# Performance work log

Measured on AMD Instinct MI355X. Metric: run time of the kernel, lower is better.

Reference implementation:

```python
import jax, jax.numpy as jnp
import numpy as np

NUM_LAYERS = 2
HIDDEN = 512
INPUT = 512


def _lstm_cell(x, h, c, Wih, Whh, bih, bbh):
    # PyTorch LSTMCell: gates ordered i, f, g, o
    g = x @ Wih.T + bih + h @ Whh.T + bbh  # [B, 4H]
    i, f, gg, o = jnp.split(g, 4, axis=-1)
    c_new = jax.nn.sigmoid(f) * c + jax.nn.sigmoid(i) * jnp.tanh(gg)
    h_new = jax.nn.sigmoid(o) * jnp.tanh(c_new)
    return h_new, c_new


def setup_inputs() -> dict:
    key = jax.random.key(0)
    ks = jax.random.split(key, 8)
    B, T = 64, 512
    s = 1.0 / np.sqrt(HIDDEN)
    return {
        "x": jax.random.normal(ks[0], (B, T, INPUT), dtype=jnp.float32),
        "h0": jax.random.normal(ks[1], (NUM_LAYERS, B, HIDDEN), dtype=jnp.float32),
        "c0": jax.random.normal(ks[2], (NUM_LAYERS, B, HIDDEN), dtype=jnp.float32),
        # stacked per-layer weights (input_size == hidden_size so shapes match)
        "W_ih": jax.random.uniform(ks[3], (NUM_LAYERS, 4 * HIDDEN, INPUT), jnp.float32, -s, s),
        "W_hh": jax.random.uniform(ks[4], (NUM_LAYERS, 4 * HIDDEN, HIDDEN), jnp.float32, -s, s),
        "b_ih": jax.random.uniform(ks[5], (NUM_LAYERS, 4 * HIDDEN), jnp.float32, -s, s),
        "b_hh": jax.random.uniform(ks[6], (NUM_LAYERS, 4 * HIDDEN), jnp.float32, -s, s),
    }


def reference(x, h0, c0, W_ih, W_hh, b_ih, b_hh):
    # x: [B, T, D]; h0/c0: [L, B, H]
    xs = jnp.swapaxes(x, 0, 1)  # [T, B, D] for scan over time

    def step(carry, x_t):
        h, c = carry  # each [L, B, H]
        h_list, c_list = [], []
        inp = x_t
        for j in range(NUM_LAYERS):  # small static unroll over layers
            h_j, c_j = _lstm_cell(inp, h[j], c[j], W_ih[j], W_hh[j], b_ih[j], b_hh[j])
            h_list.append(h_j)
            c_list.append(c_j)
            inp = h_j
        h_new = jnp.stack(h_list, axis=0)
        c_new = jnp.stack(c_list, axis=0)
        return (h_new, c_new), inp  # output of top layer

    (h_fin, c_fin), outs = jax.lax.scan(step, (h0, c0), xs)
    out = jnp.swapaxes(outs, 0, 1)  # [B, T, H]
    return out, h_fin, c_fin
```

## Files before the change

kernel.cpp:

```cpp
#include <hip/hip_runtime.h>
#include <hip/hip_bf16.h>


#define TT 512

using short8 = __attribute__((ext_vector_type(8))) short;
using f32x4  = __attribute__((ext_vector_type(4))) float;

__device__ __forceinline__ short f2bf(float f) {
  unsigned u = __float_as_uint(f);
  u = (u + 0x7fffu + ((u >> 16) & 1u)) >> 16;
  return (short)u;
}
__device__ __forceinline__ float bf2f(short s) {
  return __uint_as_float(((unsigned)(unsigned short)s) << 16);
}
__device__ __forceinline__ float sigf(float x) { return 1.f / (1.f + __expf(-x)); }
__device__ __forceinline__ float tanh_(float x) { return 1.f - 2.f / (__expf(2.f * x) + 1.f); }

__device__ __forceinline__ void ld8_nw(short8* d,
    const short* p0, const short* p1, const short* p2, const short* p3,
    const short* p4, const short* p5, const short* p6, const short* p7) {
  asm volatile(
      "global_load_dwordx4 %0, %8, off sc0\n\t"
      "global_load_dwordx4 %1, %9, off sc0\n\t"
      "global_load_dwordx4 %2, %10, off sc0\n\t"
      "global_load_dwordx4 %3, %11, off sc0\n\t"
      "global_load_dwordx4 %4, %12, off sc0\n\t"
      "global_load_dwordx4 %5, %13, off sc0\n\t"
      "global_load_dwordx4 %6, %14, off sc0\n\t"
      "global_load_dwordx4 %7, %15, off sc0"
      : "=&v"(d[0]), "=&v"(d[1]), "=&v"(d[2]), "=&v"(d[3]),
        "=&v"(d[4]), "=&v"(d[5]), "=&v"(d[6]), "=&v"(d[7])
      : "v"(p0), "v"(p1), "v"(p2), "v"(p3),
        "v"(p4), "v"(p5), "v"(p6), "v"(p7)
      : "memory");
}

#define TIE8(A, CNT)                                                        \
  asm volatile(CNT : "+v"(A[0]), "+v"(A[1]), "+v"(A[2]), "+v"(A[3]),        \
                     "+v"(A[4]), "+v"(A[5]), "+v"(A[6]), "+v"(A[7])         \
               ::"memory")

__device__ __forceinline__ void stc_short(short* p, short v) {
  asm volatile("global_store_short %0, %1, off sc0 sc1"
               :: "v"(p), "v"((int)v) : "memory");
}
__device__ __forceinline__ void stc_float(float* p, float v) {
  asm volatile("global_store_dword %0, %1, off sc0 sc1"
               :: "v"(p), "v"(v) : "memory");
}

__device__ __forceinline__ void l2inv() {
  asm volatile("buffer_inv sc1" ::: "memory");
}

__global__ __launch_bounds__(256) void conv_x(const float* __restrict__ x,
                                              short* __restrict__ xo) {
  size_t g = (size_t)blockIdx.x * 256 + threadIdx.x;
  size_t i = g * 8;
  float4 v0 = *(const float4*)(x + i);
  float4 v1 = *(const float4*)(x + i + 4);
  short8 r;
  r[0] = f2bf(v0.x); r[1] = f2bf(v0.y); r[2] = f2bf(v0.z); r[3] = f2bf(v0.w);
  r[4] = f2bf(v1.x); r[5] = f2bf(v1.y); r[6] = f2bf(v1.z); r[7] = f2bf(v1.w);
  *(short8*)(xo + (i >> 9) * 1024 + (i & 511)) = r;
}

__global__ __launch_bounds__(256) void conv_w(const float* __restrict__ Wih,
                                              const float* __restrict__ Whh,
                                              short* __restrict__ wp) {
  int g = blockIdx.x * 256 + threadIdx.x;
  int l = g / 393216;
  int rem = g % 393216;
  int j8 = rem / 6144;
  int q8 = rem % 6144;
  int s, hl, bt, c, lane;
  if (q8 < 2048) {
    s = 0; hl = 0;
    int seg = q8 >> 6; bt = seg >> 4; c = seg & 15; lane = q8 & 63;
  } else {
    int q = q8 - 2048;
    s = 1;
    int seg = q >> 6; bt = seg >> 5; c = (seg >> 1) & 15; hl = seg & 1;
    lane = q & 63;
  }
  int r = lane & 15;
  int gg = r >> 2, jj = r & 3;
  int R = gg * 512 + j8 * 8 + bt * 4 + jj;
  int k = c * 32 + (lane >> 4) * 8;
  const float* src = (s ? Whh : Wih) + ((size_t)(l * 2048 + R)) * 512 + k;
  short8 o;
#pragma unroll
  for (int e = 0; e < 8; ++e) {
    float v = src[e];
    short hi = f2bf(v);
    o[e] = hl ? f2bf(v - bf2f(hi)) : hi;
  }
  *(short8*)(wp + (size_t)g * 8) = o;
}

__global__ __launch_bounds__(256) void init_state(const float* __restrict__ h0,
                                                  short* __restrict__ hhi,
                                                  short* __restrict__ hlo,
                                                  unsigned* __restrict__ bar) {
  int i = blockIdx.x * 256 + threadIdx.x;
  int l = i >> 15, bj = i & 32767;
  int b = bj >> 9, j = bj & 511;
  float h = h0[i];
  short hi = f2bf(h);
  int slot = l ? 5 : 3;
  int o = slot * 32768 + (j >> 3) * 512 + b * 8 + (j & 7);
  hhi[o] = hi;
  hlo[o] = f2bf(h - bf2f(hi));
  if (blockIdx.x < 8) bar[blockIdx.x * 256 + threadIdx.x] = 0u;
}

__device__ __forceinline__ void garrive(unsigned* cnt, int tid, int slot) {
  __syncthreads();
  if (tid == 0)
    __hip_atomic_fetch_add(&cnt[slot * 32], 1u, __ATOMIC_RELAXED,
                           __HIP_MEMORY_SCOPE_AGENT);
}
__device__ __forceinline__ void gwait1(unsigned* c1, unsigned t1, int tid) {
  if (tid == 0) {
    for (;;) {
      unsigned s1 = 0;
#pragma unroll
      for (int r = 0; r < 32; ++r)
        s1 += __hip_atomic_load(&c1[r * 32], __ATOMIC_RELAXED,
                                __HIP_MEMORY_SCOPE_AGENT);
      if (s1 >= t1) break;
      __builtin_amdgcn_s_sleep(1);
    }
  }
  __syncthreads();
  if (tid < 64) l2inv();
  __syncthreads();
}
__device__ __forceinline__ void gwait2(unsigned* c1, unsigned t1,
                                       unsigned* c2, unsigned t2, int tid) {
  if (tid == 0) {
    for (;;) {
      unsigned s1 = 0, s2 = 0;
#pragma unroll
      for (int r = 0; r < 32; ++r) {
        s1 += __hip_atomic_load(&c1[r * 32], __ATOMIC_RELAXED,
                                __HIP_MEMORY_SCOPE_AGENT);
        s2 += __hip_atomic_load(&c2[r * 32], __ATOMIC_RELAXED,
                                __HIP_MEMORY_SCOPE_AGENT);
      }
      if (s1 >= t1 && s2 >= t2) break;
      __builtin_amdgcn_s_sleep(1);
    }
  }
  __syncthreads();
  if (tid < 64) l2inv();
  __syncthreads();
}

__global__ __launch_bounds__(512, 1) void lstm_persist(
    const short* __restrict__ wp, const float* __restrict__ c0,
    const float* __restrict__ bih, const float* __restrict__ bhh,
    short* __restrict__ hhi, short* __restrict__ hlo,
    unsigned* __restrict__ bar, float* __restrict__ out) {
  extern __shared__ char smem[];
  short* lw = (short*)smem;
  float* sG = (float*)(smem + 98304);

  const int tid = threadIdx.x;
  const int layer = blockIdx.x >> 6;
  const int j8 = blockIdx.x & 63;
  const int bslot = blockIdx.x & 31;
  unsigned* cntMy = bar + (layer << 10);
  unsigned* cntOt = bar + ((layer ^ 1) << 10);
  const int wv = tid >> 6;
  const int kq = wv & 3;
  const int ah = wv >> 2;
  const int lane = tid & 63;
  const int m = lane & 15;
  const int koq = lane >> 4;
  const int cbase = kq << 2;

  {
    const short* src = wp + (size_t)(layer * 64 + j8) * 49152;
    for (int i = tid; i < 6144; i += 512)
      *(short8*)(lw + i * 8) = *(const short8*)(src + i * 8);
  }

  const int sb = tid >> 3, sj = tid & 7;
  const int j = (j8 << 3) + sj;
  float creg = c0[layer * 32768 + sb * 512 + j];
  float hf = 0.f;
  float bsum[4];
#pragma unroll
  for (int g = 0; g < 4; ++g)
    bsum[g] = bih[layer * 2048 + g * 512 + j] + bhh[layer * 2048 + g * 512 + j];
  __syncthreads();

  const int br0 = ((ah * 2 + 0) << 4) + m;
  const int br1 = ((ah * 2 + 1) << 4) + m;
  const short* xo = (const short*)out;

  f32x4 acc[2][2];

  auto zacc = [&]() {
#pragma unroll
    for (int u = 0; u < 2; ++u)
#pragma unroll
      for (int v = 0; v < 2; ++v) acc[u][v] = f32x4{0.f, 0.f, 0.f, 0.f};
  };

#define PA(rX, cc, br) \
  ((rX) + ((((cbase + (cc)) << 2) + koq) << 9) + (br) * 8)

  auto ih_l0 = [&](int txt) {
#pragma unroll
    for (int cc = 0; cc < 4; ++cc) {
      const int c = cbase + cc;
      const int k = c * 32 + (koq << 3);
      short8 b0 = *(const short8*)(lw + c * 512 + lane * 8);
      short8 b1 = *(const short8*)(lw + (16 + c) * 512 + lane * 8);
#pragma unroll
      for (int it = 0; it < 2; ++it) {
        const int br = it ? br1 : br0;
        short8 a = *(const short8*)(xo + ((size_t)br * TT + txt) * 1024 + k);
        acc[0][it] = __builtin_amdgcn_mfma_f32_16x16x32_bf16(a, b0, acc[0][it], 0, 0, 0);
        acc[1][it] = __builtin_amdgcn_mfma_f32_16x16x32_bf16(a, b1, acc[1][it], 0, 0, 0);
      }
    }
  };

  auto ih_l1 = [&](const short* ph) {
    short8 Ax[8];
    ld8_nw(Ax, PA(ph, 0, br0), PA(ph, 0, br1), PA(ph, 1, br0), PA(ph, 1, br1),
               PA(ph, 2, br0), PA(ph, 2, br1), PA(ph, 3, br0), PA(ph, 3, br1));
    TIE8(Ax, "s_waitcnt vmcnt(0)");
#pragma unroll
    for (int cc = 0; cc < 4; ++cc) {
      const int c = cbase + cc;
      short8 b0 = *(const short8*)(lw + c * 512 + lane * 8);
      short8 b1 = *(const short8*)(lw + (16 + c) * 512 + lane * 8);
#pragma unroll
      for (int it = 0; it < 2; ++it) {
        short8 a = Ax[cc * 2 + it];
        acc[0][it] = __builtin_amdgcn_mfma_f32_16x16x32_bf16(a, b0, acc[0][it], 0, 0, 0);
        acc[1][it] = __builtin_amdgcn_mfma_f32_16x16x32_bf16(a, b1, acc[1][it], 0, 0, 0);
      }
    }
  };

  auto stepBody = [&](const short* rh, const short* rl, int slotOut, int t) {
    short8 Ah[8], Al[8];
    ld8_nw(Ah, PA(rh, 0, br0), PA(rh, 0, br1), PA(rh, 1, br0), PA(rh, 1, br1),
               PA(rh, 2, br0), PA(rh, 2, br1), PA(rh, 3, br0), PA(rh, 3, br1));
    ld8_nw(Al, PA(rl, 0, br0), PA(rl, 0, br1), PA(rl, 1, br0), PA(rl, 1, br1),
               PA(rl, 2, br0), PA(rl, 2, br1), PA(rl, 3, br0), PA(rl, 3, br1));
    TIE8(Ah, "s_waitcnt vmcnt(0)");
    TIE8(Al, "");

#pragma unroll
    for (int cc = 0; cc < 4; ++cc) {
      const int c = cbase + cc;
      short8 bh0 = *(const short8*)(lw + 16384 + (c * 2 + 0) * 512 + lane * 8);
      short8 bl0 = *(const short8*)(lw + 16384 + (c * 2 + 1) * 512 + lane * 8);
      short8 bh1 = *(const short8*)(lw + 16384 + ((16 + c) * 2 + 0) * 512 + lane * 8);
      short8 bl1 = *(const short8*)(lw + 16384 + ((16 + c) * 2 + 1) * 512 + lane * 8);
#pragma unroll
      for (int it = 0; it < 2; ++it) {
        short8 a = Ah[cc * 2 + it];
        short8 al = Al[cc * 2 + it];
        acc[0][it] = __builtin_amdgcn_mfma_f32_16x16x32_bf16(a, bh0, acc[0][it], 0, 0, 0);
        acc[0][it] = __builtin_amdgcn_mfma_f32_16x16x32_bf16(a, bl0, acc[0][it], 0, 0, 0);
        acc[0][it] = __builtin_amdgcn_mfma_f32_16x16x32_bf16(al, bh0, acc[0][it], 0, 0, 0);
        acc[1][it] = __builtin_amdgcn_mfma_f32_16x16x32_bf16(a, bh1, acc[1][it], 0, 0, 0);
        acc[1][it] = __builtin_amdgcn_mfma_f32_16x16x32_bf16(a, bl1, acc[1][it], 0, 0, 0);
        acc[1][it] = __builtin_amdgcn_mfma_f32_16x16x32_bf16(al, bh1, acc[1][it], 0, 0, 0);
      }
    }

#pragma unroll
    for (int bt = 0; bt < 2; ++bt)
#pragma unroll
      for (int it = 0; it < 2; ++it) {
        const int srow = bt * 16 + m;
        const int col = ((ah * 2 + it) << 4) + (koq << 2);
#pragma unroll
        for (int r = 0; r < 4; ++r)
          sG[(kq * 32 + srow) * 66 + col + r] = acc[bt][it][r];
      }
    __syncthreads();

    {
      const int bt = sj >> 2, jl = sj & 3;
      float gv[4];
#pragma unroll
      for (int g = 0; g < 4; ++g) {
        const int s = bt * 16 + g * 4 + jl;
        gv[g] = sG[(0 * 32 + s) * 66 + sb] + sG[(1 * 32 + s) * 66 + sb] +
                sG[(2 * 32 + s) * 66 + sb] + sG[(3 * 32 + s) * 66 + sb] +
                bsum[g];
      }
      const float cn = sigf(gv[1]) * creg + sigf(gv[0]) * tanh_(gv[2]);
      const float hn = sigf(gv[3]) * tanh_(cn);
      creg = cn;
      hf = hn;
      const int ho = slotOut * 32768 + (j8 << 9) + tid;
      const short hb = f2bf(hn);
      stc_short(hhi + ho, hb);
      stc_short(hlo + ho, f2bf(hn - bf2f(hb)));
      if (layer)
        stc_float(&out[((size_t)sb * 512 + t) * 512 + j], hn);
    }
  };

  if (layer == 0) {
    zacc();
    ih_l0(0);
    for (int t = 0; t < TT; ++t) {
      if (t >= 4)
        gwait2(cntMy, (unsigned)(64 * t), cntOt, (unsigned)(64 * (t - 3)), tid);
      else if (t >= 1)
        gwait1(cntMy, (unsigned)(64 * t), tid);
      const int ps = (t + 3) & 3;
      stepBody(hhi + ps * 32768, hlo + ps * 32768, t & 3, t);
      garrive(cntMy, tid, bslot);
      if (t + 1 < TT) {
        zacc();
        ih_l0(t + 1);
      }
    }
  } else {
    zacc();
    gwait1(cntOt, 64u, tid);
    ih_l1(hhi + 0 * 32768);
    for (int t = 0; t < TT; ++t) {
      if (t >= 1) gwait1(cntMy, (unsigned)(64 * t), tid);
      const int ps = 4 + ((t + 1) & 1);
      stepBody(hhi + ps * 32768, hlo + ps * 32768, 4 + (t & 1), t);
      garrive(cntMy, tid, bslot);
      if (t + 1 < TT) {
        gwait1(cntOt, (unsigned)(64 * (t + 2)), tid);
        zacc();
        ih_l1(hhi + ((t + 1) & 3) * 32768);
      }
    }
  }

  stc_float(&out[16777216 + layer * 32768 + sb * 512 + j], hf);
  stc_float(&out[16777216 + 65536 + layer * 32768 + sb * 512 + j], creg);
}


extern "C" void kernel_launch(void* const* d_in, const int* in_sizes, int n_in,
                              void* d_out, int out_size, void* d_ws,
                              size_t ws_size, hipStream_t stream) {
  const float* x = (const float*)d_in[0];
  const float* h0 = (const float*)d_in[1];
  const float* c0 = (const float*)d_in[2];
  const float* Wih = (const float*)d_in[3];
  const float* Whh = (const float*)d_in[4];
  const float* bih = (const float*)d_in[5];
  const float* bhh = (const float*)d_in[6];
  float* out = (float*)d_out;

  char* ws = (char*)d_ws;
  short* wp = (short*)(ws + 0);
  short* hhi = (short*)(ws + 12582912);
  short* hlo = (short*)(ws + 12976128);
  unsigned* bar = (unsigned*)(ws + 13369344);

  hipFuncSetAttribute(reinterpret_cast<const void*>(lstm_persist),
                      hipFuncAttributeMaxDynamicSharedMemorySize, 132096);

  conv_x<<<8192, 256, 0, stream>>>(x, (short*)out);
  conv_w<<<3072, 256, 0, stream>>>(Wih, Whh, wp);
  init_state<<<256, 256, 0, stream>>>(h0, hhi, hlo, bar);

  void* args[] = {(void*)&wp,  (void*)&c0,  (void*)&bih, (void*)&bhh,
                  (void*)&hhi, (void*)&hlo, (void*)&bar, (void*)&out};
  hipLaunchCooperativeKernel(reinterpret_cast<void*>(lstm_persist), dim3(128),
                             dim3(512), args, 132096, stream);
}
```

Measured before the change: 3.153 ms.

## Elect one leader block per XCC to invalidate L2 and signal peers via flags

```diff
diff --git a/kernel.cpp b/kernel.cpp
--- a/kernel.cpp
+++ b/kernel.cpp
@@ -51,8 +51,8 @@
                :: "v"(p), "v"(v) : "memory");
 }
 
-__device__ __forceinline__ void l2inv() {
-  asm volatile("buffer_inv sc1" ::: "memory");
+__device__ __forceinline__ void l2inv_wait() {
+  asm volatile("buffer_inv sc1\n\ts_waitcnt vmcnt(0)" ::: "memory");
 }
 
 __global__ __launch_bounds__(256) void conv_x(const float* __restrict__ x,
@@ -113,7 +113,16 @@
   int o = slot * 32768 + (j >> 3) * 512 + b * 8 + (j & 7);
   hhi[o] = hi;
   hlo[o] = f2bf(h - bf2f(hi));
-  if (blockIdx.x < 8) bar[blockIdx.x * 256 + threadIdx.x] = 0u;
+  if (blockIdx.x < 16) bar[blockIdx.x * 256 + threadIdx.x] = 0u;
+}
+
+__device__ __forceinline__ unsigned csum(unsigned* c) {
+  unsigned s = 0;
+#pragma unroll
+  for (int r = 0; r < 32; ++r)
+    s += __hip_atomic_load(&c[r * 32], __ATOMIC_RELAXED,
+                           __HIP_MEMORY_SCOPE_AGENT);
+  return s;
 }
 
 __device__ __forceinline__ void garrive(unsigned* cnt, int tid, int slot) {
@@ -122,40 +131,41 @@
     __hip_atomic_fetch_add(&cnt[slot * 32], 1u, __ATOMIC_RELAXED,
                            __HIP_MEMORY_SCOPE_AGENT);
 }
-__device__ __forceinline__ void gwait1(unsigned* c1, unsigned t1, int tid) {
+
+__device__ __forceinline__ void gw_main(unsigned* c1, unsigned t1,
+                                        unsigned* c2, unsigned t2, int tid,
+                                        bool lead, unsigned* flg, unsigned ft) {
   if (tid == 0) {
     for (;;) {
-      unsigned s1 = 0;
-#pragma unroll
-      for (int r = 0; r < 32; ++r)
-        s1 += __hip_atomic_load(&c1[r * 32], __ATOMIC_RELAXED,
-                                __HIP_MEMORY_SCOPE_AGENT);
-      if (s1 >= t1) break;
+      bool ok = (csum(c1) >= t1);
+      if (c2) ok = ok && (csum(c2) >= t2);
+      if (ok) break;
       __builtin_amdgcn_s_sleep(1);
     }
+    if (lead) {
+      l2inv_wait();
+      __hip_atomic_store(flg, ft, __ATOMIC_RELAXED, __HIP_MEMORY_SCOPE_AGENT);
+    } else {
+      while (__hip_atomic_load(flg, __ATOMIC_RELAXED,
+                               __HIP_MEMORY_SCOPE_AGENT) < ft)
+        __builtin_amdgcn_s_sleep(1);
+    }
   }
   __syncthreads();
-  if (tid < 64) l2inv();
-  __syncthreads();
-}
-__device__ __forceinline__ void gwait2(unsigned* c1, unsigned t1,
-                                       unsigned* c2, unsigned t2, int tid) {
+}
+
+__device__ __forceinline__ void gw_other(unsigned* c, unsigned tc, int tid,
+                                         unsigned* flg, unsigned ft) {
   if (tid == 0) {
-    for (;;) {
-      unsigned s1 = 0, s2 = 0;
-#pragma unroll
-      for (int r = 0; r < 32; ++r) {
-        s1 += __hip_atomic_load(&c1[r * 32], __ATOMIC_RELAXED,
-                                __HIP_MEMORY_SCOPE_AGENT);
-        s2 += __hip_atomic_load(&c2[r * 32], __ATOMIC_RELAXED,
-                                __HIP_MEMORY_SCOPE_AGENT);
-      }
-      if (s1 >= t1 && s2 >= t2) break;
-      __builtin_amdgcn_s_sleep(1);
-    }
-  }
-  __syncthreads();
-  if (tid < 64) l2inv();
+    while (csum(c) < tc) __builtin_amdgcn_s_sleep(1);
+    if (flg) {
+      while (__hip_atomic_load(flg, __ATOMIC_RELAXED,
+                               __HIP_MEMORY_SCOPE_AGENT) < ft)
+        __builtin_amdgcn_s_sleep(1);
+    } else {
+      l2inv_wait();
+    }
+  }
   __syncthreads();
 }
 
@@ -172,8 +182,11 @@
   const int layer = blockIdx.x >> 6;
   const int j8 = blockIdx.x & 63;
   const int bslot = blockIdx.x & 31;
-  unsigned* cntMy = bar + (layer << 10);
-  unsigned* cntOt = bar + ((layer ^ 1) << 10);
+  unsigned* cnt0 = bar;
+  unsigned* cnt1 = bar + 1024;
+  unsigned* icnt = bar + 2048;
+  unsigned* claim = bar + 2080;
+  unsigned* flags = bar + 2176;
   const int wv = tid >> 6;
   const int kq = wv & 3;
   const int ah = wv >> 2;
@@ -182,6 +195,18 @@
   const int koq = lane >> 4;
   const int cbase = kq << 2;
 
+  int xcc;
+  asm volatile("s_getreg_b32 %0, hwreg(HW_REG_XCC_ID)" : "=s"(xcc));
+  xcc &= 15;
+  bool lead = false;
+  if (tid == 0)
+    lead = (__hip_atomic_fetch_add(&claim[layer * 16 + xcc], 1u,
+                                   __ATOMIC_RELAXED,
+                                   __HIP_MEMORY_SCOPE_AGENT) == 0u);
+  if (tid == 0)
+    __hip_atomic_fetch_add(icnt, 1u, __ATOMIC_RELAXED,
+                           __HIP_MEMORY_SCOPE_AGENT);
+
   {
     const short* src = wp + (size_t)(layer * 64 + j8) * 49152;
     for (int i = tid; i < 6144; i += 512)
@@ -196,7 +221,18 @@
 #pragma unroll
   for (int g = 0; g < 4; ++g)
     bsum[g] = bih[layer * 2048 + g * 512 + j] + bhh[layer * 2048 + g * 512 + j];
+
+  unsigned cl0 = 0;
+  if (tid == 0) {
+    while (__hip_atomic_load(icnt, __ATOMIC_RELAXED,
+                             __HIP_MEMORY_SCOPE_AGENT) < 128u)
+      __builtin_amdgcn_s_sleep(1);
+    cl0 = __hip_atomic_load(&claim[0 * 16 + xcc], __ATOMIC_RELAXED,
+                            __HIP_MEMORY_SCOPE_AGENT);
+  }
   __syncthreads();
+  unsigned* myflg = flags + (layer * 16 + xcc) * 32;
+  unsigned* f0 = flags + (0 * 16 + xcc) * 32;
 
   const int br0 = ((ah * 2 + 0) << 4) + m;
   const int br1 = ((ah * 2 + 1) << 4) + m;
@@ -319,12 +355,14 @@
     ih_l0(0);
     for (int t = 0; t < TT; ++t) {
       if (t >= 4)
-        gwait2(cntMy, (unsigned)(64 * t), cntOt, (unsigned)(64 * (t - 3)), tid);
+        gw_main(cnt0, 64u * (unsigned)t, cnt1, 64u * (unsigned)(t - 3), tid,
+                lead, myflg, (unsigned)t);
       else if (t >= 1)
-        gwait1(cntMy, (unsigned)(64 * t), tid);
+        gw_main(cnt0, 64u * (unsigned)t, nullptr, 0u, tid, lead, myflg,
+                (unsigned)t);
       const int ps = (t + 3) & 3;
       stepBody(hhi + ps * 32768, hlo + ps * 32768, t & 3, t);
-      garrive(cntMy, tid, bslot);
+      garrive(cnt0, tid, bslot);
       if (t + 1 < TT) {
         zacc();
         ih_l0(t + 1);
@@ -332,15 +370,18 @@
     }
   } else {
     zacc();
-    gwait1(cntOt, 64u, tid);
+    gw_other(cnt0, 64u, tid, cl0 ? f0 : (unsigned*)nullptr, 1u);
     ih_l1(hhi + 0 * 32768);
     for (int t = 0; t < TT; ++t) {
-      if (t >= 1) gwait1(cntMy, (unsigned)(64 * t), tid);
+      if (t >= 1)
+        gw_main(cnt1, 64u * (unsigned)t, nullptr, 0u, tid, lead, myflg,
+                (unsigned)t);
       const int ps = 4 + ((t + 1) & 1);
       stepBody(hhi + ps * 32768, hlo + ps * 32768, 4 + (t & 1), t);
-      garrive(cntMy, tid, bslot);
+      garrive(cnt1, tid, bslot);
       if (t + 1 < TT) {
-        gwait1(cntOt, (unsigned)(64 * (t + 2)), tid);
+        unsigned* fx = (cl0 && (t + 2) < TT) ? f0 : (unsigned*)nullptr;
+        gw_other(cnt0, 64u * (unsigned)(t + 2), tid, fx, (unsigned)(t + 2));
         zacc();
         ih_l1(hhi + ((t + 1) & 3) * 32768);
       }
```

New measurement: 3.043 ms. -3.5%, faster.

## Deepen hidden-state ring to 16 slots and skip per-step L2 invalidation

Applied to the files above, without the earlier changes.

```diff
diff --git a/kernel.cpp b/kernel.cpp
--- a/kernel.cpp
+++ b/kernel.cpp
@@ -18,7 +18,7 @@
 __device__ __forceinline__ float sigf(float x) { return 1.f / (1.f + __expf(-x)); }
 __device__ __forceinline__ float tanh_(float x) { return 1.f - 2.f / (__expf(2.f * x) + 1.f); }
 
-__device__ __forceinline__ void ld8_nw(short8* d,
+__device__ __forceinline__ void ld8_c(short8* d,
     const short* p0, const short* p1, const short* p2, const short* p3,
     const short* p4, const short* p5, const short* p6, const short* p7) {
   asm volatile(
@@ -30,6 +30,25 @@
       "global_load_dwordx4 %5, %13, off sc0\n\t"
       "global_load_dwordx4 %6, %14, off sc0\n\t"
       "global_load_dwordx4 %7, %15, off sc0"
+      : "=&v"(d[0]), "=&v"(d[1]), "=&v"(d[2]), "=&v"(d[3]),
+        "=&v"(d[4]), "=&v"(d[5]), "=&v"(d[6]), "=&v"(d[7])
+      : "v"(p0), "v"(p1), "v"(p2), "v"(p3),
+        "v"(p4), "v"(p5), "v"(p6), "v"(p7)
+      : "memory");
+}
+
+__device__ __forceinline__ void ld8_d(short8* d,
+    const short* p0, const short* p1, const short* p2, const short* p3,
+    const short* p4, const short* p5, const short* p6, const short* p7) {
+  asm volatile(
+      "global_load_dwordx4 %0, %8, off sc0 sc1\n\t"
+      "global_load_dwordx4 %1, %9, off sc0 sc1\n\t"
+      "global_load_dwordx4 %2, %10, off sc0 sc1\n\t"
+      "global_load_dwordx4 %3, %11, off sc0 sc1\n\t"
+      "global_load_dwordx4 %4, %12, off sc0 sc1\n\t"
+      "global_load_dwordx4 %5, %13, off sc0 sc1\n\t"
+      "global_load_dwordx4 %6, %14, off sc0 sc1\n\t"
+      "global_load_dwordx4 %7, %15, off sc0 sc1"
       : "=&v"(d[0]), "=&v"(d[1]), "=&v"(d[2]), "=&v"(d[3]),
         "=&v"(d[4]), "=&v"(d[5]), "=&v"(d[6]), "=&v"(d[7])
       : "v"(p0), "v"(p1), "v"(p2), "v"(p3),
@@ -109,11 +128,20 @@
   int b = bj >> 9, j = bj & 511;
   float h = h0[i];
   short hi = f2bf(h);
-  int slot = l ? 5 : 3;
+  int slot = l ? 31 : 15;
   int o = slot * 32768 + (j >> 3) * 512 + b * 8 + (j & 7);
   hhi[o] = hi;
   hlo[o] = f2bf(h - bf2f(hi));
   if (blockIdx.x < 8) bar[blockIdx.x * 256 + threadIdx.x] = 0u;
+}
+
+__device__ __forceinline__ unsigned csum(unsigned* c) {
+  unsigned s = 0;
+#pragma unroll
+  for (int r = 0; r < 32; ++r)
+    s += __hip_atomic_load(&c[r * 32], __ATOMIC_RELAXED,
+                           __HIP_MEMORY_SCOPE_AGENT);
+  return s;
 }
 
 __device__ __forceinline__ void garrive(unsigned* cnt, int tid, int slot) {
@@ -122,40 +150,38 @@
     __hip_atomic_fetch_add(&cnt[slot * 32], 1u, __ATOMIC_RELAXED,
                            __HIP_MEMORY_SCOPE_AGENT);
 }
-__device__ __forceinline__ void gwait1(unsigned* c1, unsigned t1, int tid) {
+
+__device__ __forceinline__ void gwait1(unsigned* c1, unsigned t1, int tid,
+                                       bool doinv) {
+  if (tid == 0) {
+    while (csum(c1) < t1) __builtin_amdgcn_s_sleep(1);
+  }
+  __syncthreads();
+  if (doinv) {
+    if (tid < 64) l2inv();
+    __syncthreads();
+  }
+}
+__device__ __forceinline__ void gwait2(unsigned* c1, unsigned t1,
+                                       unsigned* c2, unsigned t2, int tid,
+                                       bool doinv) {
   if (tid == 0) {
     for (;;) {
-      unsigned s1 = 0;
-#pragma unroll
-      for (int r = 0; r < 32; ++r)
-        s1 += __hip_atomic_load(&c1[r * 32], __ATOMIC_RELAXED,
-                                __HIP_MEMORY_SCOPE_AGENT);
-      if (s1 >= t1) break;
+      if (csum(c1) >= t1 && csum(c2) >= t2) break;
       __builtin_amdgcn_s_sleep(1);
     }
   }
   __syncthreads();
-  if (tid < 64) l2inv();
-  __syncthreads();
-}
-__device__ __forceinline__ void gwait2(unsigned* c1, unsigned t1,
-                                       unsigned* c2, unsigned t2, int tid) {
+  if (doinv) {
+    if (tid < 64) l2inv();
+    __syncthreads();
+  }
+}
+
+__device__ __forceinline__ void gw_other(unsigned* c, unsigned tc, int tid) {
   if (tid == 0) {
-    for (;;) {
-      unsigned s1 = 0, s2 = 0;
-#pragma unroll
-      for (int r = 0; r < 32; ++r) {
-        s1 += __hip_atomic_load(&c1[r * 32], __ATOMIC_RELAXED,
-                                __HIP_MEMORY_SCOPE_AGENT);
-        s2 += __hip_atomic_load(&c2[r * 32], __ATOMIC_RELAXED,
-                                __HIP_MEMORY_SCOPE_AGENT);
-      }
-      if (s1 >= t1 && s2 >= t2) break;
-      __builtin_amdgcn_s_sleep(1);
-    }
-  }
-  __syncthreads();
-  if (tid < 64) l2inv();
+    while (csum(c) < tc) __builtin_amdgcn_s_sleep(1);
+  }
   __syncthreads();
 }
 
@@ -172,8 +198,8 @@
   const int layer = blockIdx.x >> 6;
   const int j8 = blockIdx.x & 63;
   const int bslot = blockIdx.x & 31;
-  unsigned* cntMy = bar + (layer << 10);
-  unsigned* cntOt = bar + ((layer ^ 1) << 10);
+  unsigned* cnt0 = bar;
+  unsigned* cnt1 = bar + 1024;
   const int wv = tid >> 6;
   const int kq = wv & 3;
   const int ah = wv >> 2;
@@ -233,8 +259,8 @@
 
   auto ih_l1 = [&](const short* ph) {
     short8 Ax[8];
-    ld8_nw(Ax, PA(ph, 0, br0), PA(ph, 0, br1), PA(ph, 1, br0), PA(ph, 1, br1),
-               PA(ph, 2, br0), PA(ph, 2, br1), PA(ph, 3, br0), PA(ph, 3, br1));
+    ld8_d(Ax, PA(ph, 0, br0), PA(ph, 0, br1), PA(ph, 1, br0), PA(ph, 1, br1),
+              PA(ph, 2, br0), PA(ph, 2, br1), PA(ph, 3, br0), PA(ph, 3, br1));
     TIE8(Ax, "s_waitcnt vmcnt(0)");
 #pragma unroll
     for (int cc = 0; cc < 4; ++cc) {
@@ -252,10 +278,10 @@
 
   auto stepBody = [&](const short* rh, const short* rl, int slotOut, int t) {
     short8 Ah[8], Al[8];
-    ld8_nw(Ah, PA(rh, 0, br0), PA(rh, 0, br1), PA(rh, 1, br0), PA(rh, 1, br1),
-               PA(rh, 2, br0), PA(rh, 2, br1), PA(rh, 3, br0), PA(rh, 3, br1));
-    ld8_nw(Al, PA(rl, 0, br0), PA(rl, 0, br1), PA(rl, 1, br0), PA(rl, 1, br1),
-               PA(rl, 2, br0), PA(rl, 2, br1), PA(rl, 3, br0), PA(rl, 3, br1));
+    ld8_c(Ah, PA(rh, 0, br0), PA(rh, 0, br1), PA(rh, 1, br0), PA(rh, 1, br1),
+              PA(rh, 2, br0), PA(rh, 2, br1), PA(rh, 3, br0), PA(rh, 3, br1));
+    ld8_c(Al, PA(rl, 0, br0), PA(rl, 0, br1), PA(rl, 1, br0), PA(rl, 1, br1),
+              PA(rl, 2, br0), PA(rl, 2, br1), PA(rl, 3, br0), PA(rl, 3, br1));
     TIE8(Ah, "s_waitcnt vmcnt(0)");
     TIE8(Al, "");
 
@@ -318,13 +344,14 @@
     zacc();
     ih_l0(0);
     for (int t = 0; t < TT; ++t) {
-      if (t >= 4)
-        gwait2(cntMy, (unsigned)(64 * t), cntOt, (unsigned)(64 * (t - 3)), tid);
+      if (t >= 16)
+        gwait2(cnt0, 64u * (unsigned)t, cnt1, 64u * (unsigned)(t - 15), tid,
+               (t & 15) == 0);
       else if (t >= 1)
-        gwait1(cntMy, (unsigned)(64 * t), tid);
-      const int ps = (t + 3) & 3;
-      stepBody(hhi + ps * 32768, hlo + ps * 32768, t & 3, t);
-      garrive(cntMy, tid, bslot);
+        gwait1(cnt0, 64u * (unsigned)t, tid, false);
+      const int ps = (t + 15) & 15;
+      stepBody(hhi + ps * 32768, hlo + ps * 32768, t & 15, t);
+      garrive(cnt0, tid, bslot);
       if (t + 1 < TT) {
         zacc();
         ih_l0(t + 1);
@@ -332,17 +359,18 @@
     }
   } else {
     zacc();
-    gwait1(cntOt, 64u, tid);
+    gw_other(cnt0, 64u, tid);
     ih_l1(hhi + 0 * 32768);
     for (int t = 0; t < TT; ++t) {
-      if (t >= 1) gwait1(cntMy, (unsigned)(64 * t), tid);
-      const int ps = 4 + ((t + 1) & 1);
-      stepBody(hhi + ps * 32768, hlo + ps * 32768, 4 + (t & 1), t);
-      garrive(cntMy, tid, bslot);
+      if (t >= 1)
+        gwait1(cnt1, 64u * (unsigned)t, tid, ((t & 15) == 0) && t >= 16);
+      const int ps = 16 + ((t + 15) & 15);
+      stepBody(hhi + ps * 32768, hlo + ps * 32768, 16 + (t & 15), t);
+      garrive(cnt1, tid, bslot);
       if (t + 1 < TT) {
-        gwait1(cntOt, (unsigned)(64 * (t + 2)), tid);
+        gw_other(cnt0, 64u * (unsigned)(t + 2), tid);
         zacc();
-        ih_l1(hhi + ((t + 1) & 3) * 32768);
+        ih_l1(hhi + ((t + 1) & 15) * 32768);
       }
     }
   }
@@ -367,8 +395,8 @@
   char* ws = (char*)d_ws;
   short* wp = (short*)(ws + 0);
   short* hhi = (short*)(ws + 12582912);
-  short* hlo = (short*)(ws + 12976128);
-  unsigned* bar = (unsigned*)(ws + 13369344);
+  short* hlo = (short*)(ws + 14680064);
+  unsigned* bar = (unsigned*)(ws + 16777216);
 
   hipFuncSetAttribute(reinterpret_cast<const void*>(lstm_persist),
                       hipFuncAttributeMaxDynamicSharedMemorySize, 132096);
```

Result: faster. 2.837 ms (-10.0%).

## Replace counter barriers with tag-polled packed hidden-state ring buffer

Applied to the files above, without the earlier changes.

```diff
diff --git a/kernel.cpp b/kernel.cpp
--- a/kernel.cpp
+++ b/kernel.cpp
@@ -6,6 +6,7 @@
 
 using short8 = __attribute__((ext_vector_type(8))) short;
 using f32x4  = __attribute__((ext_vector_type(4))) float;
+using u32x4  = __attribute__((ext_vector_type(4))) unsigned;
 
 __device__ __forceinline__ short f2bf(float f) {
   unsigned u = __float_as_uint(f);
@@ -17,42 +18,54 @@
 }
 __device__ __forceinline__ float sigf(float x) { return 1.f / (1.f + __expf(-x)); }
 __device__ __forceinline__ float tanh_(float x) { return 1.f - 2.f / (__expf(2.f * x) + 1.f); }
-
-__device__ __forceinline__ void ld8_nw(short8* d,
-    const short* p0, const short* p1, const short* p2, const short* p3,
-    const short* p4, const short* p5, const short* p6, const short* p7) {
+__device__ __forceinline__ unsigned ETAG(int t) {
+  return ((unsigned)(t + 16) >> 4) & 3u;
+}
+
+__device__ __forceinline__ void ld16p(u32x4* R,
+    const unsigned* p0, const unsigned* p1, const unsigned* p2,
+    const unsigned* p3, const unsigned* p4, const unsigned* p5,
+    const unsigned* p6, const unsigned* p7) {
   asm volatile(
-      "global_load_dwordx4 %0, %8, off sc0\n\t"
-      "global_load_dwordx4 %1, %9, off sc0\n\t"
-      "global_load_dwordx4 %2, %10, off sc0\n\t"
-      "global_load_dwordx4 %3, %11, off sc0\n\t"
-      "global_load_dwordx4 %4, %12, off sc0\n\t"
-      "global_load_dwordx4 %5, %13, off sc0\n\t"
-      "global_load_dwordx4 %6, %14, off sc0\n\t"
-      "global_load_dwordx4 %7, %15, off sc0"
-      : "=&v"(d[0]), "=&v"(d[1]), "=&v"(d[2]), "=&v"(d[3]),
-        "=&v"(d[4]), "=&v"(d[5]), "=&v"(d[6]), "=&v"(d[7])
+      "global_load_dwordx4 %0, %16, off sc0 sc1\n\t"
+      "global_load_dwordx4 %1, %16, off offset:16 sc0 sc1\n\t"
+      "global_load_dwordx4 %2, %17, off sc0 sc1\n\t"
+      "global_load_dwordx4 %3, %17, off offset:16 sc0 sc1\n\t"
+      "global_load_dwordx4 %4, %18, off sc0 sc1\n\t"
+      "global_load_dwordx4 %5, %18, off offset:16 sc0 sc1\n\t"
+      "global_load_dwordx4 %6, %19, off sc0 sc1\n\t"
+      "global_load_dwordx4 %7, %19, off offset:16 sc0 sc1\n\t"
+      "global_load_dwordx4 %8, %20, off sc0 sc1\n\t"
+      "global_load_dwordx4 %9, %20, off offset:16 sc0 sc1\n\t"
+      "global_load_dwordx4 %10, %21, off sc0 sc1\n\t"
+      "global_load_dwordx4 %11, %21, off offset:16 sc0 sc1\n\t"
+      "global_load_dwordx4 %12, %22, off sc0 sc1\n\t"
+      "global_load_dwordx4 %13, %22, off offset:16 sc0 sc1\n\t"
+      "global_load_dwordx4 %14, %23, off sc0 sc1\n\t"
+      "global_load_dwordx4 %15, %23, off offset:16 sc0 sc1"
+      : "=&v"(R[0]), "=&v"(R[1]), "=&v"(R[2]), "=&v"(R[3]),
+        "=&v"(R[4]), "=&v"(R[5]), "=&v"(R[6]), "=&v"(R[7]),
+        "=&v"(R[8]), "=&v"(R[9]), "=&v"(R[10]), "=&v"(R[11]),
+        "=&v"(R[12]), "=&v"(R[13]), "=&v"(R[14]), "=&v"(R[15])
       : "v"(p0), "v"(p1), "v"(p2), "v"(p3),
         "v"(p4), "v"(p5), "v"(p6), "v"(p7)
       : "memory");
 }
 
-#define TIE8(A, CNT)                                                        \
+#define TIE16(A, CNT)                                                       \
   asm volatile(CNT : "+v"(A[0]), "+v"(A[1]), "+v"(A[2]), "+v"(A[3]),        \
-                     "+v"(A[4]), "+v"(A[5]), "+v"(A[6]), "+v"(A[7])         \
+                     "+v"(A[4]), "+v"(A[5]), "+v"(A[6]), "+v"(A[7]),        \
+                     "+v"(A[8]), "+v"(A[9]), "+v"(A[10]), "+v"(A[11]),      \
+                     "+v"(A[12]), "+v"(A[13]), "+v"(A[14]), "+v"(A[15])     \
                ::"memory")
 
-__device__ __forceinline__ void stc_short(short* p, short v) {
-  asm volatile("global_store_short %0, %1, off sc0 sc1"
-               :: "v"(p), "v"((int)v) : "memory");
+__device__ __forceinline__ void stc_dword(unsigned* p, unsigned v) {
+  asm volatile("global_store_dword %0, %1, off sc0 sc1"
+               :: "v"(p), "v"(v) : "memory");
 }
 __device__ __forceinline__ void stc_float(float* p, float v) {
   asm volatile("global_store_dword %0, %1, off sc0 sc1"
                :: "v"(p), "v"(v) : "memory");
-}
-
-__device__ __forceinline__ void l2inv() {
-  asm volatile("buffer_inv sc1" ::: "memory");
 }
 
 __global__ __launch_bounds__(256) void conv_x(const float* __restrict__ x,
@@ -101,69 +114,62 @@
 }
 
 __global__ __launch_bounds__(256) void init_state(const float* __restrict__ h0,
-                                                  short* __restrict__ hhi,
-                                                  short* __restrict__ hlo,
+                                                  unsigned* __restrict__ hp,
                                                   unsigned* __restrict__ bar) {
-  int i = blockIdx.x * 256 + threadIdx.x;
-  int l = i >> 15, bj = i & 32767;
-  int b = bj >> 9, j = bj & 511;
-  float h = h0[i];
-  short hi = f2bf(h);
-  int slot = l ? 5 : 3;
-  int o = slot * 32768 + (j >> 3) * 512 + b * 8 + (j & 7);
-  hhi[o] = hi;
-  hlo[o] = f2bf(h - bf2f(hi));
+  unsigned idx = blockIdx.x * 256 + threadIdx.x;
+  int slot = idx >> 15;
+  unsigned w = idx & 32767u;
+  unsigned word = 0u;
+  if (slot == 15 || slot == 31) {
+    int l = slot >> 4;
+    int k8 = w >> 9, b = (w >> 3) & 63, e = w & 7;
+    int j = k8 * 8 + e;
+    float h = h0[l * 32768 + b * 512 + j];
+    short hi = f2bf(h);
+    unsigned lo = (unsigned)(unsigned short)f2bf(h - bf2f(hi));
+    lo = (lo + 2u) & 0xFFFCu;
+    word = ((unsigned)(unsigned short)hi << 16) | lo;
+  }
+  hp[idx] = word;
   if (blockIdx.x < 8) bar[blockIdx.x * 256 + threadIdx.x] = 0u;
 }
 
+__device__ __forceinline__ unsigned csum(unsigned* c) {
+  unsigned s = 0;
+#pragma unroll
+  for (int r = 0; r < 32; ++r)
+    s += __hip_atomic_load(&c[r * 32], __ATOMIC_RELAXED,
+                           __HIP_MEMORY_SCOPE_AGENT);
+  return s;
+}
 __device__ __forceinline__ void garrive(unsigned* cnt, int tid, int slot) {
   __syncthreads();
   if (tid == 0)
     __hip_atomic_fetch_add(&cnt[slot * 32], 1u, __ATOMIC_RELAXED,
                            __HIP_MEMORY_SCOPE_AGENT);
 }
-__device__ __forceinline__ void gwait1(unsigned* c1, unsigned t1, int tid) {
+__device__ __forceinline__ void guard1(unsigned* c1, unsigned t1, int tid) {
   if (tid == 0) {
-    for (;;) {
-      unsigned s1 = 0;
-#pragma unroll
-      for (int r = 0; r < 32; ++r)
-        s1 += __hip_atomic_load(&c1[r * 32], __ATOMIC_RELAXED,
-                                __HIP_MEMORY_SCOPE_AGENT);
-      if (s1 >= t1) break;
-      __builtin_amdgcn_s_sleep(1);
-    }
+    while (csum(c1) < t1) __builtin_amdgcn_s_sleep(1);
   }
   __syncthreads();
-  if (tid < 64) l2inv();
-  __syncthreads();
-}
-__device__ __forceinline__ void gwait2(unsigned* c1, unsigned t1,
+}
+__device__ __forceinline__ void guard2(unsigned* c1, unsigned t1,
                                        unsigned* c2, unsigned t2, int tid) {
   if (tid == 0) {
     for (;;) {
-      unsigned s1 = 0, s2 = 0;
-#pragma unroll
-      for (int r = 0; r < 32; ++r) {
-        s1 += __hip_atomic_load(&c1[r * 32], __ATOMIC_RELAXED,
-                                __HIP_MEMORY_SCOPE_AGENT);
-        s2 += __hip_atomic_load(&c2[r * 32], __ATOMIC_RELAXED,
-                                __HIP_MEMORY_SCOPE_AGENT);
-      }
-      if (s1 >= t1 && s2 >= t2) break;
+      if (csum(c1) >= t1 && csum(c2) >= t2) break;
       __builtin_amdgcn_s_sleep(1);
     }
   }
-  __syncthreads();
-  if (tid < 64) l2inv();
   __syncthreads();
 }
 
 __global__ __launch_bounds__(512, 1) void lstm_persist(
     const short* __restrict__ wp, const float* __restrict__ c0,
     const float* __restrict__ bih, const float* __restrict__ bhh,
-    short* __restrict__ hhi, short* __restrict__ hlo,
-    unsigned* __restrict__ bar, float* __restrict__ out) {
+    unsigned* __restrict__ hp, unsigned* __restrict__ bar,
+    float* __restrict__ out) {
   extern __shared__ char smem[];
   short* lw = (short*)smem;
   float* sG = (float*)(smem + 98304);
@@ -172,8 +178,8 @@
   const int layer = blockIdx.x >> 6;
   const int j8 = blockIdx.x & 63;
   const int bslot = blockIdx.x & 31;
-  unsigned* cntMy = bar + (layer << 10);
-  unsigned* cntOt = bar + ((layer ^ 1) << 10);
+  unsigned* cnt0 = bar;
+  unsigned* cnt1 = bar + 1024;
   const int wv = tid >> 6;
   const int kq = wv & 3;
   const int ah = wv >> 2;
@@ -211,8 +217,22 @@
       for (int v = 0; v < 2; ++v) acc[u][v] = f32x4{0.f, 0.f, 0.f, 0.f};
   };
 
-#define PA(rX, cc, br) \
+#define PAU(rX, cc, br) \
   ((rX) + ((((cbase + (cc)) << 2) + koq) << 9) + (br) * 8)
+
+  auto pollLoad = [&](u32x4* R, const unsigned* rp, unsigned et) {
+    for (;;) {
+      ld16p(R, PAU(rp, 0, br0), PAU(rp, 0, br1), PAU(rp, 1, br0),
+               PAU(rp, 1, br1), PAU(rp, 2, br0), PAU(rp, 2, br1),
+               PAU(rp, 3, br0), PAU(rp, 3, br1));
+      TIE16(R, "s_waitcnt vmcnt(0)");
+      int ok = 1;
+#pragma unroll
+      for (int i = 0; i < 8; ++i) ok &= ((R[2 * i][0] & 3u) == et) ? 1 : 0;
+      if (__all(ok)) break;
+      __builtin_amdgcn_s_sleep(1);
+    }
+  };
 
   auto ih_l0 = [&](int txt) {
 #pragma unroll
@@ -231,11 +251,9 @@
     }
   };
 
-  auto ih_l1 = [&](const short* ph) {
-    short8 Ax[8];
-    ld8_nw(Ax, PA(ph, 0, br0), PA(ph, 0, br1), PA(ph, 1, br0), PA(ph, 1, br1),
-               PA(ph, 2, br0), PA(ph, 2, br1), PA(ph, 3, br0), PA(ph, 3, br1));
-    TIE8(Ax, "s_waitcnt vmcnt(0)");
+  auto ih_l1 = [&](const unsigned* rp, unsigned et) {
+    u32x4 R[16];
+    pollLoad(R, rp, et);
 #pragma unroll
     for (int cc = 0; cc < 4; ++cc) {
       const int c = cbase + cc;
@@ -243,21 +261,40 @@
       short8 b1 = *(const short8*)(lw + (16 + c) * 512 + lane * 8);
 #pragma unroll
       for (int it = 0; it < 2; ++it) {
-        short8 a = Ax[cc * 2 + it];
-        acc[0][it] = __builtin_amdgcn_mfma_f32_16x16x32_bf16(a, b0, acc[0][it], 0, 0, 0);
-        acc[1][it] = __builtin_amdgcn_mfma_f32_16x16x32_bf16(a, b1, acc[1][it], 0, 0, 0);
+        const int i = cc * 2 + it;
+        u32x4 a = R[2 * i], b = R[2 * i + 1];
+        u32x4 H;
+        H[0] = (a[1] & 0xFFFF0000u) | (a[0] >> 16);
+        H[1] = (a[3] & 0xFFFF0000u) | (a[2] >> 16);
+        H[2] = (b[1] & 0xFFFF0000u) | (b[0] >> 16);
+        H[3] = (b[3] & 0xFFFF0000u) | (b[2] >> 16);
+        short8 Ax = *(short8*)&H;
+        acc[0][it] = __builtin_amdgcn_mfma_f32_16x16x32_bf16(Ax, b0, acc[0][it], 0, 0, 0);
+        acc[1][it] = __builtin_amdgcn_mfma_f32_16x16x32_bf16(Ax, b1, acc[1][it], 0, 0, 0);
       }
     }
   };
 
-  auto stepBody = [&](const short* rh, const short* rl, int slotOut, int t) {
+  auto stepBody = [&](const unsigned* rp, int slotOut, int t, unsigned etR,
+                      unsigned tagW) {
+    u32x4 R[16];
+    pollLoad(R, rp, etR);
     short8 Ah[8], Al[8];
-    ld8_nw(Ah, PA(rh, 0, br0), PA(rh, 0, br1), PA(rh, 1, br0), PA(rh, 1, br1),
-               PA(rh, 2, br0), PA(rh, 2, br1), PA(rh, 3, br0), PA(rh, 3, br1));
-    ld8_nw(Al, PA(rl, 0, br0), PA(rl, 0, br1), PA(rl, 1, br0), PA(rl, 1, br1),
-               PA(rl, 2, br0), PA(rl, 2, br1), PA(rl, 3, br0), PA(rl, 3, br1));
-    TIE8(Ah, "s_waitcnt vmcnt(0)");
-    TIE8(Al, "");
+#pragma unroll
+    for (int i = 0; i < 8; ++i) {
+      u32x4 a = R[2 * i], b = R[2 * i + 1];
+      u32x4 H, L;
+      H[0] = (a[1] & 0xFFFF0000u) | (a[0] >> 16);
+      H[1] = (a[3] & 0xFFFF0000u) | (a[2] >> 16);
+      H[2] = (b[1] & 0xFFFF0000u) | (b[0] >> 16);
+      H[3] = (b[3] & 0xFFFF0000u) | (b[2] >> 16);
+      L[0] = (a[1] << 16) | (a[0] & 0xFFFFu);
+      L[1] = (a[3] << 16) | (a[2] & 0xFFFFu);
+      L[2] = (b[1] << 16) | (b[0] & 0xFFFFu);
+      L[3] = (b[3] << 16) | (b[2] & 0xFFFFu);
+      Ah[i] = *(short8*)&H;
+      Al[i] = *(short8*)&L;
+    }
 
 #pragma unroll
     for (int cc = 0; cc < 4; ++cc) {
@@ -305,10 +342,11 @@
       const float hn = sigf(gv[3]) * tanh_(cn);
       creg = cn;
       hf = hn;
-      const int ho = slotOut * 32768 + (j8 << 9) + tid;
       const short hb = f2bf(hn);
-      stc_short(hhi + ho, hb);
-      stc_short(hlo + ho, f2bf(hn - bf2f(hb)));
+      unsigned lo = (unsigned)(unsigned short)f2bf(hn - bf2f(hb));
+      lo = ((lo + 2u) & 0xFFFCu) | tagW;
+      const unsigned word = ((unsigned)(unsigned short)hb << 16) | lo;
+      stc_dword(hp + slotOut * 32768 + (j8 << 9) + tid, word);
       if (layer)
         stc_float(&out[((size_t)sb * 512 + t) * 512 + j], hn);
     }
@@ -318,13 +356,11 @@
     zacc();
     ih_l0(0);
     for (int t = 0; t < TT; ++t) {
-      if (t >= 4)
-        gwait2(cntMy, (unsigned)(64 * t), cntOt, (unsigned)(64 * (t - 3)), tid);
-      else if (t >= 1)
-        gwait1(cntMy, (unsigned)(64 * t), tid);
-      const int ps = (t + 3) & 3;
-      stepBody(hhi + ps * 32768, hlo + ps * 32768, t & 3, t);
-      garrive(cntMy, tid, bslot);
+      if (t >= 16)
+        guard2(cnt0, 64u * (unsigned)(t - 15), cnt1, 64u * (unsigned)(t - 15),
+               tid);
+      stepBody(hp + ((t + 15) & 15) * 32768, t & 15, t, ETAG(t - 1), ETAG(t));
+      garrive(cnt0, tid, bslot);
       if (t + 1 < TT) {
         zacc();
         ih_l0(t + 1);
@@ -332,17 +368,16 @@
     }
   } else {
     zacc();
-    gwait1(cntOt, 64u, tid);
-    ih_l1(hhi + 0 * 32768);
+    ih_l1(hp + 0 * 32768, ETAG(0));
     for (int t = 0; t < TT; ++t) {
-      if (t >= 1) gwait1(cntMy, (unsigned)(64 * t), tid);
-      const int ps = 4 + ((t + 1) & 1);
-      stepBody(hhi + ps * 32768, hlo + ps * 32768, 4 + (t & 1), t);
-      garrive(cntMy, tid, bslot);
+      if (t >= 16)
+        guard1(cnt1, 64u * (unsigned)(t - 15), tid);
+      stepBody(hp + (16 + ((t + 15) & 15)) * 32768, 16 + (t & 15), t,
+               ETAG(t - 1), ETAG(t));
+      garrive(cnt1, tid, bslot);
       if (t + 1 < TT) {
-        gwait1(cntOt, (unsigned)(64 * (t + 2)), tid);
         zacc();
-        ih_l1(hhi + ((t + 1) & 3) * 32768);
+        ih_l1(hp + ((t + 1) & 15) * 32768, ETAG(t + 1));
       }
     }
   }
@@ -366,19 +401,18 @@
 
   char* ws = (char*)d_ws;
   short* wp = (short*)(ws + 0);
-  short* hhi = (short*)(ws + 12582912);
-  short* hlo = (short*)(ws + 12976128);
-  unsigned* bar = (unsigned*)(ws + 13369344);
+  unsigned* hp = (unsigned*)(ws + 12582912);
+  unsigned* bar = (unsigned*)(ws + 16777216);
 
   hipFuncSetAttribute(reinterpret_cast<const void*>(lstm_persist),
                       hipFuncAttributeMaxDynamicSharedMemorySize, 132096);
 
   conv_x<<<8192, 256, 0, stream>>>(x, (short*)out);
   conv_w<<<3072, 256, 0, stream>>>(Wih, Whh, wp);
-  init_state<<<256, 256, 0, stream>>>(h0, hhi, hlo, bar);
-
-  void* args[] = {(void*)&wp,  (void*)&c0,  (void*)&bih, (void*)&bhh,
-                  (void*)&hhi, (void*)&hlo, (void*)&bar, (void*)&out};
-  hipLaunchCooperativeKernel(reinterpret_cast<void*>(lstm_persist), dim3(128),
-                             dim3(512), args, 132096, stream);
-}
+  init_state<<<4096, 256, 0, stream>>>(h0, hp, bar);
+
+  void* args[] = {(void*)&wp, (void*)&c0,  (void*)&bih, (void*)&bhh,
+                  (void*)&hp, (void*)&bar, (void*)&out};
+  (void)hipLaunchCooperativeKernel(reinterpret_cast<void*>(lstm_persist),
+                                   dim3(128), dim3(512), args, 132096, stream);
+}
```

Measured after the change: 3.109 ms. No clear change (-1.4%).
